# Performance work log

Measured on AMD Instinct MI355X. Metric: run time of the kernel, lower is better.

The kernel has to match this reference:

```python
import jax, jax.numpy as jnp
import numpy as np

M_HIST = 5        # Anderson history depth (m=5 in anderson_solver)
N_POWER = 20      # power iterations to estimate sigma for spectral_norm
REG = 1e-4        # Tikhonov regularization on the Anderson LS system
MAX_ITER = 25     # deq_max_iter


def _l2norm(x):
    return x / (jnp.linalg.norm(x) + 1e-12)


def spectral_normalize(W):
    # torch spectral_norm: W / sigma, sigma = u^T W v with u,v from power iteration
    u = _l2norm(jnp.ones((W.shape[0],), W.dtype))
    def body(_, u):
        v = _l2norm(W.T @ u)
        return _l2norm(W @ v)
    u = jax.lax.fori_loop(0, N_POWER, body, u)
    v = _l2norm(W.T @ u)
    u = jax.lax.stop_gradient(u)
    v = jax.lax.stop_gradient(v)
    sigma = u @ (W @ v)
    return W / sigma


def make_f(W1, b1, W2, b2):
    W1s = spectral_normalize(W1)
    W2s = spectral_normalize(W2)
    def f(z, context):
        h = jnp.tanh(jnp.concatenate([z, context], axis=-1) @ W1s.T + b1)
        return jnp.tanh(h @ W2s.T + b2)
    return f


def anderson(f, x0, context, max_iter, m=M_HIST):
    # Mirrors anderson_solver, including its duplicated warm-up step.
    X = [x0]
    F = [f(x0, context)]
    x = F[0]; X.append(x); F.append(f(x, context))
    x = F[0]; X.append(x); F.append(f(x, context))
    for _k in range(2, max_iter):
        m_k = min(len(X) - 1, m)
        dX = jnp.stack([X[-i] - X[-i - 1] for i in range(1, m_k + 1)], axis=-1)  # [B,d,mk]
        dF = jnp.stack([F[-i] - F[-i - 1] for i in range(1, m_k + 1)], axis=-1)
        dG = dF - dX
        A = jnp.einsum('bdi,bdj->bij', dG, dG) + REG * jnp.eye(m_k, dtype=x0.dtype)
        r = F[-1] - X[-1]
        Bv = jnp.einsum('bdi,bd->bi', dG, r)
        alpha = jnp.linalg.solve(A, Bv[..., None])[..., 0]          # [B,mk]
        x = F[-1] - jnp.einsum('bdi,bi->bd', dF, alpha)
        X.append(x)
        F.append(f(x, context))
        if len(X) > m + 1:
            X.pop(0); F.pop(0)
    return X[-1]


def setup_inputs() -> dict:
    key = jax.random.key(0)
    ks = jax.random.split(key, 5)
    B, X_DIM, LATENT, HIDDEN = 2048, 256, 256, 1024
    context = jax.random.normal(ks[0], (B, X_DIM), jnp.float32)
    W1 = jax.random.normal(ks[1], (HIDDEN, LATENT + X_DIM), jnp.float32) / np.sqrt(LATENT + X_DIM)
    b1 = jax.random.normal(ks[2], (HIDDEN,), jnp.float32) * 0.01
    W2 = jax.random.normal(ks[3], (LATENT, HIDDEN), jnp.float32) / np.sqrt(HIDDEN)
    b2 = jax.random.normal(ks[4], (LATENT,), jnp.float32) * 0.01
    return {"context": context, "W1": W1, "b1": b1, "W2": W2, "b2": b2}


def reference(context, W1, b1, W2, b2):
    f = make_f(W1, b1, W2, b2)
    z0 = jnp.zeros((context.shape[0], W2.shape[0]), context.dtype)
    z_star = anderson(f, z0, context, MAX_ITER)
    return z_star
```

## Files before the change

### kernel.cpp

```cpp
#include <hip/hip_runtime.h>
#include <hip/hip_bf16.h>


#define B_ROWS 2048
#define D_LAT  256
#define D_CTX  256
#define D_HID  1024
#define KCAT   512
#define SLOT   (B_ROWS * D_LAT)
#define NRING  7

typedef __bf16 bf16x8 __attribute__((ext_vector_type(8)));
typedef float f32x4 __attribute__((ext_vector_type(4)));
typedef float f32x2 __attribute__((ext_vector_type(2)));
typedef unsigned short u16;

__global__ void init_kernel(const float* __restrict__ ctx,
                            __hip_bfloat16* __restrict__ zc,
                            float* __restrict__ vA, float* __restrict__ uA,
                            float* __restrict__ G1p, float* __restrict__ G2,
                            float* __restrict__ Xh) {
  int i = blockIdx.x * 256 + threadIdx.x;
  if (i < B_ROWS * KCAT) {
    int b = i >> 9, c = i & 511;
    float v = (c < 256) ? 0.0f : ctx[b * 256 + (c - 256)];
    zc[i] = __float2bfloat16(v);
  }
  if (i < SLOT) Xh[i] = 0.0f;
  if (i < 512 * 512) G1p[i] = 0.0f;
  if (i < 256 * 256) G2[i] = 0.0f;
  if (i < KCAT) vA[i] = 0.0f;
  if (i < D_LAT) uA[i] = 1.0f;
}

__global__ __launch_bounds__(256) void gram_kernel(
    const float* __restrict__ W1, const float* __restrict__ W2,
    float* __restrict__ G1p, float* __restrict__ G2,
    float* __restrict__ vA) {
  __shared__ float As[32][66];
  __shared__ float Bs[32][34];
  const int tid = threadIdx.x;
  const int tx = tid & 15, ty = tid >> 4;

  int b = blockIdx.x;
  if (b >= 1280) {
    int cb = b - 1280;
    for (int c = tid; c < KCAT; c += 256) {
      float s = 0.f;
#pragma unroll
      for (int r = 0; r < 16; r++) s += W1[(size_t)(16 * cb + r) * KCAT + c];
      atomicAdd(&vA[c], s);
    }
    return;
  }

  const float* X; float* G; int N, ti, tj, k0base; bool modeA;
  if (b < 1024) {
    modeA = true; X = W1; G = G1p; N = 512;
    int s = b >> 7, t = b & 127;
    ti = t >> 4; tj = t & 15; k0base = s * 128;
  } else {
    modeA = false; b -= 1024; X = W2; G = G2; N = 256;
    int s = b >> 5, t = b & 31;
    ti = t >> 3; tj = t & 7; k0base = s * 128;
  }

  float acc[4][2] = {};
  for (int k0 = k0base; k0 < k0base + 128; k0 += 32) {
    if (modeA) {
      for (int idx = tid; idx < 1024; idx += 256) {
        int r2 = (idx & 31) * 2, c = idx >> 5;
        f32x2 v = *(const f32x2*)(X + (size_t)(k0 + c) * 512 + ti * 64 + r2);
        *(f32x2*)&As[c][r2] = v;
      }
      for (int idx = tid; idx < 512; idx += 256) {
        int r2 = (idx & 15) * 2, c = idx >> 4;
        f32x2 v = *(const f32x2*)(X + (size_t)(k0 + c) * 512 + tj * 32 + r2);
        *(f32x2*)&Bs[c][r2] = v;
      }
    } else {
      for (int idx = tid; idx < 1024; idx += 256) {
        int c2 = (idx & 15) * 2, r = idx >> 4;
        f32x2 v = *(const f32x2*)(X + (size_t)(ti * 64 + r) * 1024 + k0 + c2);
        As[c2][r] = v[0];
        As[c2 + 1][r] = v[1];
      }
      for (int idx = tid; idx < 512; idx += 256) {
        int c2 = (idx & 15) * 2, r = idx >> 4;
        f32x2 v = *(const f32x2*)(X + (size_t)(tj * 32 + r) * 1024 + k0 + c2);
        Bs[c2][r] = v[0];
        Bs[c2 + 1][r] = v[1];
      }
    }
    __syncthreads();
#pragma unroll
    for (int kk = 0; kk < 32; kk++) {
      const float2* ap = (const float2*)&As[kk][ty * 4];
      float2 a0 = ap[0], a1 = ap[1];
      float2 b0 = *(const float2*)&Bs[kk][tx * 2];
      float a[4] = {a0.x, a0.y, a1.x, a1.y};
      float bb[2] = {b0.x, b0.y};
#pragma unroll
      for (int i = 0; i < 4; i++)
#pragma unroll
        for (int j = 0; j < 2; j++) acc[i][j] += a[i] * bb[j];
    }
    __syncthreads();
  }
#pragma unroll
  for (int i = 0; i < 4; i++)
#pragma unroll
    for (int j = 0; j < 2; j++)
      atomicAdd(&G[(size_t)(ti * 64 + ty * 4 + i) * N + tj * 32 + tx * 2 + j],
                acc[i][j]);
}

__global__ __launch_bounds__(256) void pmv_kernel(
    const float* __restrict__ G1p, const float* __restrict__ G2,
    const float* __restrict__ vi, float* __restrict__ vo,
    const float* __restrict__ ui, float* __restrict__ uo, int g1_active) {
  int gw = blockIdx.x * 4 + (threadIdx.x >> 6);
  int lane = threadIdx.x & 63;
  const float* G; const float* in; float* out; int n, r;
  if (gw < 512) {
    if (!g1_active) return;
    G = G1p; in = vi; out = vo; n = 512; r = gw;
  } else {
    G = G2; in = ui; out = uo; n = 256; r = gw - 512;
  }
  const float4* Gr = (const float4*)(G + (size_t)r * n);
  const float4* uv = (const float4*)in;
  float acc = 0.f;
  for (int c = lane; c < (n >> 2); c += 64) {
    float4 g = Gr[c], u = uv[c];
    acc += g.x * u.x + g.y * u.y + g.z * u.z + g.w * u.w;
  }
  for (int off = 32; off; off >>= 1) acc += __shfl_down(acc, off, 64);
  if (lane == 0) out[r] = 0.25f * acc;
}

__global__ __launch_bounds__(256) void sigma_kernel(
    const float* __restrict__ vA, const float* __restrict__ vB,
    const float* __restrict__ uA, const float* __restrict__ uB,
    float* __restrict__ sig) {
  float s[4] = {0.f, 0.f, 0.f, 0.f};
  for (int i = threadIdx.x; i < KCAT; i += 256) {
    s[0] += vA[i] * vB[i];
    s[1] += vA[i] * vA[i];
  }
  for (int i = threadIdx.x; i < D_LAT; i += 256) {
    s[2] += uA[i] * uA[i];
    s[3] += uA[i] * uB[i];
  }
  __shared__ float red[4][4];
  int lane = threadIdx.x & 63, w = threadIdx.x >> 6;
  for (int k = 0; k < 4; k++) {
    float a = s[k];
    for (int off = 32; off; off >>= 1) a += __shfl_down(a, off, 64);
    if (lane == 0) red[k][w] = a;
  }
  __syncthreads();
  if (threadIdx.x == 0) {
    float d0 = red[0][0] + red[0][1] + red[0][2] + red[0][3];
    float d1 = red[1][0] + red[1][1] + red[1][2] + red[1][3];
    float d2 = red[2][0] + red[2][1] + red[2][2] + red[2][3];
    float d3 = red[3][0] + red[3][1] + red[3][2] + red[3][3];
    sig[0] = sqrtf(0.25f * d0 / d1);
    sig[1] = sqrtf(0.25f * d2 / d3);
  }
}

__global__ void wfold_kernel(const float* __restrict__ W1,
                             const float* __restrict__ W2,
                             const float* __restrict__ sig,
                             __hip_bfloat16* __restrict__ W1b,
                             __hip_bfloat16* __restrict__ W2b) {
  int i = blockIdx.x * 256 + threadIdx.x;
  if (i < D_HID * KCAT) W1b[i] = __float2bfloat16(W1[i] * sig[0]);
  int j = i - D_HID * KCAT;
  if (j >= 0 && j < D_LAT * D_HID) W2b[j] = __float2bfloat16(W2[j] * sig[1]);
}

template <int BM, int BN, int K, int OUT_MODE>
__global__ __launch_bounds__(256) void gemm_mfma(
    const __hip_bfloat16* __restrict__ A, const __hip_bfloat16* __restrict__ W,
    const float* __restrict__ bias, float* __restrict__ P0,
    float* __restrict__ P1, float* __restrict__ P2,
    __hip_bfloat16* __restrict__ Cb, int N) {
  __shared__ __align__(16) u16 lds[2][(BM + BN) * 64];
  const int tid = threadIdx.x;
  const int lane = tid & 63;
  const int wid = tid >> 6;
  const int wy = wid >> 1, wx = wid & 1;
  constexpr int WM = BM / 2, WN = BN / 2;
  constexpr int MB = WM / 16, NB = WN / 16;
  constexpr int NK = K / 64;
  const int bm = blockIdx.x * BM;
  const int bn = blockIdx.y * BN;
  const int rlo = lane & 15, quad = lane >> 4;

  f32x4 acc[MB][NB] = {};

  auto stage = [&](u16* base, int k0) {
    u16* As = base;
    u16* Ws = base + BM * 64;
    for (int c = tid; c < BM * 8; c += 256) {
      int r = c >> 3, o = (c & 7) ^ (r & 7);
      __builtin_amdgcn_global_load_lds(
          (const __attribute__((address_space(1))) void*)(A + (size_t)(bm + r) * K + k0 + o * 8),
          (__attribute__((address_space(3))) void*)(As + c * 8), 16, 0, 0);
    }
    for (int c = tid; c < BN * 8; c += 256) {
      int r = c >> 3, o = (c & 7) ^ (r & 7);
      __builtin_amdgcn_global_load_lds(
          (const __attribute__((address_space(1))) void*)(W + (size_t)(bn + r) * K + k0 + o * 8),
          (__attribute__((address_space(3))) void*)(Ws + c * 8), 16, 0, 0);
    }
  };
  auto compute = [&](const u16* base) {
    const u16* As = base;
    const u16* Ws = base + BM * 64;
#pragma unroll
    for (int kk = 0; kk < 2; kk++) {
      bf16x8 af[MB], bfr[NB];
#pragma unroll
      for (int mb = 0; mb < MB; mb++) {
        int r = wy * WM + mb * 16 + rlo;
        int o = (kk * 4 + quad) ^ (r & 7);
        af[mb] = *(const bf16x8*)(As + (r * 8 + o) * 8);
      }
#pragma unroll
      for (int nb = 0; nb < NB; nb++) {
        int r = wx * WN + nb * 16 + rlo;
        int o = (kk * 4 + quad) ^ (r & 7);
        bfr[nb] = *(const bf16x8*)(Ws + (r * 8 + o) * 8);
      }
#pragma unroll
      for (int mb = 0; mb < MB; mb++)
#pragma unroll
        for (int nb = 0; nb < NB; nb++)
          acc[mb][nb] = __builtin_amdgcn_mfma_f32_16x16x32_bf16(
              af[mb], bfr[nb], acc[mb][nb], 0, 0, 0);
    }
  };

  stage(&lds[0][0], 0);
  __syncthreads();
#pragma unroll 2
  for (int step = 0; step < NK; step++) {
    u16* cur = (step & 1) ? &lds[1][0] : &lds[0][0];
    u16* nxt = (step & 1) ? &lds[0][0] : &lds[1][0];
    if (step + 1 < NK) stage(nxt, (step + 1) * 64);
    compute(cur);
    if (step + 1 < NK) __syncthreads();
  }

#pragma unroll
  for (int mb = 0; mb < MB; mb++) {
#pragma unroll
    for (int nb = 0; nb < NB; nb++) {
      int n = bn + wx * WN + nb * 16 + rlo;
      float bv = bias[n];
#pragma unroll
      for (int rg = 0; rg < 4; rg++) {
        int m = bm + wy * WM + mb * 16 + quad * 4 + rg;
        float val = tanhf(acc[mb][nb][rg] + bv);
        size_t idx = (size_t)m * N + n;
        if constexpr (OUT_MODE == 0) {
          Cb[idx] = __float2bfloat16(val);
        } else if constexpr (OUT_MODE == 1) {
          P0[idx] = val;
        } else if constexpr (OUT_MODE == 2) {
          P0[idx] = val;
          P1[idx] = val;
          P2[idx] = val;
          Cb[(size_t)m * KCAT + n] = __float2bfloat16(val);
        } else {
          P0[idx] = val;
          P1[idx] = val;
        }
      }
    }
  }
}

template <int MK>
__global__ __launch_bounds__(256) void anderson_step_kernel(
    const float* __restrict__ Xh, const float* __restrict__ Fh,
    float* __restrict__ Xw, __hip_bfloat16* __restrict__ zc, int t) {
  const int lane = threadIdx.x & 63;
  const int wid = threadIdx.x >> 6;
  const int b = blockIdx.x * 4 + wid;
  const int base = b * D_LAT + 4 * lane;

  f32x4 f[MK + 1], x[MK + 1];
#pragma unroll
  for (int i = 0; i <= MK; i++) {
    int sl = (t - 1 - i) % NRING;
    f[i] = *(const f32x4*)(Fh + (size_t)sl * SLOT + base);
    x[i] = *(const f32x4*)(Xh + (size_t)sl * SLOT + base);
  }

  const f32x4 r = f[0] - x[0];
  f32x4 dF[MK], dG[MK];
#pragma unroll
  for (int i = 0; i < MK; i++) {
    dF[i] = f[i] - f[i + 1];
    dG[i] = dF[i] - (x[i] - x[i + 1]);
  }

  constexpr int NV = MK * (MK + 1) / 2 + MK;
  float vals[NV];
  {
    int p = 0;
#pragma unroll
    for (int i = 0; i < MK; i++)
#pragma unroll
      for (int j = i; j < MK; j++) {
        f32x4 q = dG[i] * dG[j];
        vals[p++] = q[0] + q[1] + q[2] + q[3];
      }
#pragma unroll
    for (int i = 0; i < MK; i++) {
      f32x4 q = dG[i] * r;
      vals[p++] = q[0] + q[1] + q[2] + q[3];
    }
  }
#pragma unroll
  for (int off = 1; off <= 32; off <<= 1)
#pragma unroll
    for (int v = 0; v < NV; v++) vals[v] += __shfl_xor(vals[v], off, 64);

  float A[MK][MK], bv[MK], alpha[MK];
  {
    int p = 0;
#pragma unroll
    for (int i = 0; i < MK; i++)
#pragma unroll
      for (int j = i; j < MK; j++) {
        A[i][j] = vals[p];
        A[j][i] = vals[p];
        p++;
      }
#pragma unroll
    for (int i = 0; i < MK; i++) A[i][i] += 1e-4f;
#pragma unroll
    for (int i = 0; i < MK; i++) bv[i] = vals[p++];
  }

#pragma unroll
  for (int c = 0; c < MK; c++) {
    float inv = 1.0f / A[c][c];
#pragma unroll
    for (int rr = c + 1; rr < MK; rr++) {
      float fct = A[rr][c] * inv;
#pragma unroll
      for (int cc = c; cc < MK; cc++) A[rr][cc] -= fct * A[c][cc];
      bv[rr] -= fct * bv[c];
    }
  }
#pragma unroll
  for (int i = MK - 1; i >= 0; i--) {
    float s = bv[i];
#pragma unroll
    for (int j = i + 1; j < MK; j++) s -= A[i][j] * alpha[j];
    alpha[i] = s / A[i][i];
  }

  f32x4 xo = f[0];
#pragma unroll
  for (int i = 0; i < MK; i++) xo -= dF[i] * alpha[i];
  *(f32x4*)(Xw + base) = xo;
  if (zc != nullptr) {
    union { __hip_bfloat16 h[4]; unsigned long long u; } cv;
#pragma unroll
    for (int j = 0; j < 4; j++) cv.h[j] = __float2bfloat16(xo[j]);
    *(unsigned long long*)(zc + (size_t)b * KCAT + 4 * lane) = cv.u;
  }
}

extern "C" void kernel_launch(void* const* d_in, const int* in_sizes, int n_in,
                              void* d_out, int out_size, void* d_ws,
                              size_t ws_size, hipStream_t stream) {
  const float* ctx = (const float*)d_in[0];
  const float* W1 = (const float*)d_in[1];
  const float* b1 = (const float*)d_in[2];
  const float* W2 = (const float*)d_in[3];
  const float* b2 = (const float*)d_in[4];
  float* out = (float*)d_out;

  float* ws = (float*)d_ws;
  float* sig = ws;
  float* vA = ws + 16;
  float* vB = vA + KCAT;
  float* uA = vB + KCAT;
  float* uB = uA + D_LAT;
  float* G1p = uB + D_LAT;
  float* G2 = G1p + KCAT * KCAT;
  float* Xh = G2 + D_LAT * D_LAT;
  float* Fh = Xh + NRING * SLOT;
  __hip_bfloat16* W1b = (__hip_bfloat16*)(Fh + NRING * SLOT);
  __hip_bfloat16* W2b = W1b + D_HID * KCAT;
  __hip_bfloat16* zc = W2b + D_LAT * D_HID;
  __hip_bfloat16* hb = zc + B_ROWS * KCAT;

  init_kernel<<<(B_ROWS * KCAT + 255) / 256, 256, 0, stream>>>(
      ctx, zc, vA, uA, G1p, G2, Xh);
  gram_kernel<<<1344, 256, 0, stream>>>(W1, W2, G1p, G2, vA);

  for (int it = 1; it <= 21; it++) {
    const float* vi; float* vo;
    const float* ui; float* uo;
    if (it & 1) { vi = vB; vo = vA; ui = uA; uo = uB; }
    else        { vi = vA; vo = vB; ui = uB; uo = uA; }
    pmv_kernel<<<192, 256, 0, stream>>>(G1p, G2, vi, vo, ui, uo, it >= 2);
  }
  sigma_kernel<<<1, 256, 0, stream>>>(vA, vB, uA, uB, sig);
  wfold_kernel<<<(D_HID * KCAT + D_LAT * D_HID + 255) / 256, 256, 0, stream>>>(
      W1, W2, sig, W1b, W2b);

  dim3 g1(B_ROWS / 64, D_HID / 64);
  dim3 g2(B_ROWS / 32, D_LAT / 32);

  gemm_mfma<64, 64, KCAT, 0><<<g1, 256, 0, stream>>>(
      zc, W1b, b1, nullptr, nullptr, nullptr, hb, D_HID);
  gemm_mfma<32, 32, D_HID, 2><<<g2, 256, 0, stream>>>(
      hb, W2b, b2, Fh, Xh + SLOT, Xh + 2 * SLOT, zc, D_LAT);
  gemm_mfma<64, 64, KCAT, 0><<<g1, 256, 0, stream>>>(
      zc, W1b, b1, nullptr, nullptr, nullptr, hb, D_HID);
  gemm_mfma<32, 32, D_HID, 3><<<g2, 256, 0, stream>>>(
      hb, W2b, b2, Fh + SLOT, Fh + 2 * SLOT, nullptr, nullptr, D_LAT);

  for (int t = 3; t <= 25; t++) {
    int mk = (t - 1 < 5) ? (t - 1) : 5;
    float* Xw = (t == 25) ? out : (Xh + (t % NRING) * SLOT);
    __hip_bfloat16* zarg = (t == 25) ? nullptr : zc;
    dim3 g(B_ROWS / 4);
    if (mk == 2)
      anderson_step_kernel<2><<<g, 256, 0, stream>>>(Xh, Fh, Xw, zarg, t);
    else if (mk == 3)
      anderson_step_kernel<3><<<g, 256, 0, stream>>>(Xh, Fh, Xw, zarg, t);
    else if (mk == 4)
      anderson_step_kernel<4><<<g, 256, 0, stream>>>(Xh, Fh, Xw, zarg, t);
    else
      anderson_step_kernel<5><<<g, 256, 0, stream>>>(Xh, Fh, Xw, zarg, t);
    if (t < 25) {
      gemm_mfma<64, 64, KCAT, 0><<<g1, 256, 0, stream>>>(
          zc, W1b, b1, nullptr, nullptr, nullptr, hb, D_HID);
      gemm_mfma<32, 32, D_HID, 1><<<g2, 256, 0, stream>>>(
          hb, W2b, b2, Fh + (t % NRING) * SLOT, nullptr, nullptr, nullptr,
          D_LAT);
    }
  }
}
```

Baseline: 762.1 us.

## Hoist loop-invariant context projection out of the Anderson iteration GEMM

The context half of the first layer (ctx·W1_ctxᵀ + b1) is identical in every iteration. It is now computed once into an fp32 buffer `hpre`. The first iteration, where z is zero, just applies tanh to it through a new small kernel. Later first-layer GEMMs run over only the 256 latent columns (K=256 with leading dimension 512) and add `hpre` in the epilogue. This halves the MFMA work and the A/W loads per iteration, but each GEMM must now read an 8 MB fp32 pre-activation buffer, which adds memory traffic.

```diff
diff --git a/kernel.cpp b/kernel.cpp
--- a/kernel.cpp
+++ b/kernel.cpp
@@ -181,7 +181,17 @@
   if (j >= 0 && j < D_LAT * D_HID) W2b[j] = __float2bfloat16(W2[j] * sig[1]);
 }
 
-template <int BM, int BN, int K, int OUT_MODE>
+__global__ void h0_kernel(const float* __restrict__ hpre,
+                          __hip_bfloat16* __restrict__ hb) {
+  size_t i = (size_t)(blockIdx.x * 256 + threadIdx.x) * 4;
+  f32x4 v = *(const f32x4*)(hpre + i);
+  union { __hip_bfloat16 h[4]; unsigned long long u; } cv;
+#pragma unroll
+  for (int j = 0; j < 4; j++) cv.h[j] = __float2bfloat16(tanhf(v[j]));
+  *(unsigned long long*)((__hip_bfloat16*)hb + i) = cv.u;
+}
+
+template <int BM, int BN, int K, int LDA, int LDW, int OUT_MODE>
 __global__ __launch_bounds__(256) void gemm_mfma(
     const __hip_bfloat16* __restrict__ A, const __hip_bfloat16* __restrict__ W,
     const float* __restrict__ bias, float* __restrict__ P0,
@@ -207,13 +217,13 @@
     for (int c = tid; c < BM * 8; c += 256) {
       int r = c >> 3, o = (c & 7) ^ (r & 7);
       __builtin_amdgcn_global_load_lds(
-          (const __attribute__((address_space(1))) void*)(A + (size_t)(bm + r) * K + k0 + o * 8),
+          (const __attribute__((address_space(1))) void*)(A + (size_t)(bm + r) * LDA + k0 + o * 8),
           (__attribute__((address_space(3))) void*)(As + c * 8), 16, 0, 0);
     }
     for (int c = tid; c < BN * 8; c += 256) {
       int r = c >> 3, o = (c & 7) ^ (r & 7);
       __builtin_amdgcn_global_load_lds(
-          (const __attribute__((address_space(1))) void*)(W + (size_t)(bn + r) * K + k0 + o * 8),
+          (const __attribute__((address_space(1))) void*)(W + (size_t)(bn + r) * LDW + k0 + o * 8),
           (__attribute__((address_space(3))) void*)(Ws + c * 8), 16, 0, 0);
     }
   };
@@ -260,24 +270,29 @@
 #pragma unroll
     for (int nb = 0; nb < NB; nb++) {
       int n = bn + wx * WN + nb * 16 + rlo;
-      float bv = bias[n];
+      float bv = 0.f;
+      if constexpr (OUT_MODE != 4) bv = bias[n];
 #pragma unroll
       for (int rg = 0; rg < 4; rg++) {
         int m = bm + wy * WM + mb * 16 + quad * 4 + rg;
-        float val = tanhf(acc[mb][nb][rg] + bv);
         size_t idx = (size_t)m * N + n;
-        if constexpr (OUT_MODE == 0) {
-          Cb[idx] = __float2bfloat16(val);
-        } else if constexpr (OUT_MODE == 1) {
-          P0[idx] = val;
+        if constexpr (OUT_MODE == 1) {
+          P0[idx] = tanhf(acc[mb][nb][rg] + bv);
         } else if constexpr (OUT_MODE == 2) {
+          float val = tanhf(acc[mb][nb][rg] + bv);
           P0[idx] = val;
           P1[idx] = val;
           P2[idx] = val;
           Cb[(size_t)m * KCAT + n] = __float2bfloat16(val);
-        } else {
+        } else if constexpr (OUT_MODE == 3) {
+          float val = tanhf(acc[mb][nb][rg] + bv);
           P0[idx] = val;
           P1[idx] = val;
+        } else if constexpr (OUT_MODE == 4) {
+          float val = tanhf(acc[mb][nb][rg] + P1[idx]);
+          Cb[idx] = __float2bfloat16(val);
+        } else {
+          P0[idx] = acc[mb][nb][rg] + bv;
         }
       }
     }
@@ -397,7 +412,8 @@
   float* uB = uA + D_LAT;
   float* G1p = uB + D_LAT;
   float* G2 = G1p + KCAT * KCAT;
-  float* Xh = G2 + D_LAT * D_LAT;
+  float* hpre = G2 + D_LAT * D_LAT;
+  float* Xh = hpre + (size_t)B_ROWS * D_HID;
   float* Fh = Xh + NRING * SLOT;
   __hip_bfloat16* W1b = (__hip_bfloat16*)(Fh + NRING * SLOT);
   __hip_bfloat16* W2b = W1b + D_HID * KCAT;
@@ -422,13 +438,14 @@
   dim3 g1(B_ROWS / 64, D_HID / 64);
   dim3 g2(B_ROWS / 32, D_LAT / 32);
 
-  gemm_mfma<64, 64, KCAT, 0><<<g1, 256, 0, stream>>>(
-      zc, W1b, b1, nullptr, nullptr, nullptr, hb, D_HID);
-  gemm_mfma<32, 32, D_HID, 2><<<g2, 256, 0, stream>>>(
+  gemm_mfma<64, 64, 256, 512, 512, 5><<<g1, 256, 0, stream>>>(
+      zc + 256, W1b + 256, b1, hpre, nullptr, nullptr, nullptr, D_HID);
+  h0_kernel<<<B_ROWS * D_HID / 1024, 256, 0, stream>>>(hpre, hb);
+  gemm_mfma<32, 32, D_HID, D_HID, D_HID, 2><<<g2, 256, 0, stream>>>(
       hb, W2b, b2, Fh, Xh + SLOT, Xh + 2 * SLOT, zc, D_LAT);
-  gemm_mfma<64, 64, KCAT, 0><<<g1, 256, 0, stream>>>(
-      zc, W1b, b1, nullptr, nullptr, nullptr, hb, D_HID);
-  gemm_mfma<32, 32, D_HID, 3><<<g2, 256, 0, stream>>>(
+  gemm_mfma<64, 64, 256, 512, 512, 4><<<g1, 256, 0, stream>>>(
+      zc, W1b, nullptr, nullptr, hpre, nullptr, hb, D_HID);
+  gemm_mfma<32, 32, D_HID, D_HID, D_HID, 3><<<g2, 256, 0, stream>>>(
       hb, W2b, b2, Fh + SLOT, Fh + 2 * SLOT, nullptr, nullptr, D_LAT);
 
   for (int t = 3; t <= 25; t++) {
@@ -445,9 +462,9 @@
     else
       anderson_step_kernel<5><<<g, 256, 0, stream>>>(Xh, Fh, Xw, zarg, t);
     if (t < 25) {
-      gemm_mfma<64, 64, KCAT, 0><<<g1, 256, 0, stream>>>(
-          zc, W1b, b1, nullptr, nullptr, nullptr, hb, D_HID);
-      gemm_mfma<32, 32, D_HID, 1><<<g2, 256, 0, stream>>>(
+      gemm_mfma<64, 64, 256, 512, 512, 4><<<g1, 256, 0, stream>>>(
+          zc, W1b, nullptr, nullptr, hpre, nullptr, hb, D_HID);
+      gemm_mfma<32, 32, D_HID, D_HID, D_HID, 1><<<g2, 256, 0, stream>>>(
           hb, W2b, b2, Fh + (t % NRING) * SLOT, nullptr, nullptr, nullptr,
           D_LAT);
     }
```

After: 788.3 us. +3.4%, slower.
